# Optimization experiments

Hardware: AMD Instinct MI355X
Metric: run time of the kernel (lower is better)

## Reference

```python
import jax, jax.numpy as jnp
import numpy as np

B, N, DIM = 8, 1024, 768
HEADS, DHEAD = 12, 64
INNER = HEADS * DHEAD  # 768
ALPHA = 0.25
SCALE = DHEAD ** -0.5
EPS = 1e-5


def setup_inputs() -> dict:
    key = jax.random.key(0)
    ks = jax.random.split(key, 7)
    x = jax.random.normal(ks[0], (B, N, DIM), dtype=jnp.float32)
    h = jax.random.normal(ks[1], (B, HEADS, N, N), dtype=jnp.float32)
    gamma = jnp.ones((DIM,), dtype=jnp.float32)
    beta = jnp.zeros((DIM,), dtype=jnp.float32)
    w_qkv = jax.random.normal(ks[2], (DIM, 3 * INNER), dtype=jnp.float32) * (DIM ** -0.5)
    w_out = jax.random.normal(ks[3], (INNER, DIM), dtype=jnp.float32) * (INNER ** -0.5)
    b_out = jnp.zeros((DIM,), dtype=jnp.float32)
    return {"x": x, "h": h, "gamma": gamma, "beta": beta,
            "w_qkv": w_qkv, "w_out": w_out, "b_out": b_out}


def reference(x, h, gamma, beta, w_qkv, w_out, b_out):
    # LayerNorm over last dim
    mu = jnp.mean(x, axis=-1, keepdims=True)
    var = jnp.mean(jnp.square(x - mu), axis=-1, keepdims=True)
    xn = (x - mu) * jax.lax.rsqrt(var + EPS) * gamma + beta
    # fused QKV projection (no bias)
    qkv = xn @ w_qkv                                     # (b, n, 3*inner)
    q, k, v = jnp.split(qkv, 3, axis=-1)
    split_heads = lambda t: t.reshape(B, N, HEADS, DHEAD).transpose(0, 2, 1, 3)  # b h n d
    q, k, v = split_heads(q), split_heads(k), split_heads(v)
    raw = jnp.einsum('bhid,bhjd->bhij', q, k) * SCALE    # (b, h, n, n)
    blended = ALPHA * raw + (1.0 - ALPHA) * h
    attn = jax.nn.softmax(blended, axis=-1)              # dropout p=0 -> identity
    out = jnp.einsum('bhij,bhjd->bhid', attn, v)         # (b, h, n, d)
    out = out.transpose(0, 2, 1, 3).reshape(B, N, INNER)
    out = out @ w_out + b_out
    return (out, blended)
```

## Files before the change

### kernel.cpp

```cpp
#include <hip/hip_runtime.h>
#include <hip/hip_bf16.h>
#include <stdint.h>

#define NB 8
#define NSEQ 1024
#define DIMM 768
#define NHEADS 12
#define DH 64
#define NQKV 2304
#define ALPHA_ 0.25f
#define SCALE_ 0.125f
#define EPS_ 1e-5f

typedef __bf16 bf16;
typedef bf16 bf16x8 __attribute__((ext_vector_type(8)));
typedef bf16 bf16x4 __attribute__((ext_vector_type(4)));
typedef float f32x4 __attribute__((ext_vector_type(4)));

#define MFMA16(a, b, c) __builtin_amdgcn_mfma_f32_16x16x32_bf16((a), (b), (c), 0, 0, 0)

static __device__ __forceinline__ void load_lds16(const void* gsrc, void* ldst) {
  __builtin_amdgcn_global_load_lds(
      (__attribute__((address_space(1))) void*)gsrc,
      (__attribute__((address_space(3))) void*)ldst, 16, 0, 0);
}

#define BAR_LGKM()                                             \
  do {                                                         \
    __builtin_amdgcn_sched_barrier(0);                         \
    asm volatile("s_waitcnt lgkmcnt(0)" ::: "memory");         \
    __builtin_amdgcn_s_barrier();                              \
    __builtin_amdgcn_sched_barrier(0);                         \
  } while (0)

static __device__ __forceinline__ int swz(int row, int cb) {
  return cb ^ ((((row & 7) ^ ((cb >> 7) & 7)) << 4));
}

__global__ __launch_bounds__(256) void ln_kernel(
    const float* __restrict__ x, const float* __restrict__ gamma,
    const float* __restrict__ beta, bf16* __restrict__ xn) {
  const int row = blockIdx.x * 4 + (threadIdx.x >> 6);
  const int lane = threadIdx.x & 63;
  const float* xr = x + (size_t)row * DIMM;
  float4 v[3];
  float s = 0.f, s2 = 0.f;
#pragma unroll
  for (int c = 0; c < 3; ++c) {
    v[c] = *reinterpret_cast<const float4*>(xr + c * 256 + lane * 4);
    s += v[c].x + v[c].y + v[c].z + v[c].w;
    s2 += v[c].x * v[c].x + v[c].y * v[c].y + v[c].z * v[c].z + v[c].w * v[c].w;
  }
#pragma unroll
  for (int m = 1; m < 64; m <<= 1) {
    s += __shfl_xor(s, m);
    s2 += __shfl_xor(s2, m);
  }
  const float mu = s * (1.f / DIMM);
  const float rstd = rsqrtf(s2 * (1.f / DIMM) - mu * mu + EPS_);
#pragma unroll
  for (int c = 0; c < 3; ++c) {
    const float4 g4 = *reinterpret_cast<const float4*>(gamma + c * 256 + lane * 4);
    const float4 b4 = *reinterpret_cast<const float4*>(beta + c * 256 + lane * 4);
    bf16x4 o;
    o[0] = (bf16)((v[c].x - mu) * rstd * g4.x + b4.x);
    o[1] = (bf16)((v[c].y - mu) * rstd * g4.y + b4.y);
    o[2] = (bf16)((v[c].z - mu) * rstd * g4.z + b4.z);
    o[3] = (bf16)((v[c].w - mu) * rstd * g4.w + b4.w);
    *reinterpret_cast<bf16x4*>(xn + (size_t)row * DIMM + c * 256 + lane * 4) = o;
  }
}

__global__ __launch_bounds__(256) void tcast_kernel(
    const float* __restrict__ in, bf16* __restrict__ out, int R, int C) {
  __shared__ float tile[32][33];
  const int tx = threadIdx.x & 31, ty = threadIdx.x >> 5;
  const int c0 = blockIdx.x * 32, r0 = blockIdx.y * 32;
#pragma unroll
  for (int i = ty; i < 32; i += 8)
    tile[i][tx] = in[(size_t)(r0 + i) * C + c0 + tx];
  __syncthreads();
#pragma unroll
  for (int i = ty; i < 32; i += 8)
    out[(size_t)(c0 + i) * R + r0 + tx] = (bf16)tile[tx][i];
}

__global__ __launch_bounds__(256) void qkv_gemm(
    const bf16* __restrict__ xn, const bf16* __restrict__ wT,
    bf16* __restrict__ qb, bf16* __restrict__ kb, bf16* __restrict__ vt) {
  __shared__ __align__(16) bf16 As[128 * 32];
  __shared__ __align__(16) bf16 Bs[64 * 32];
  const int tid = threadIdx.x;
  const int wv = tid >> 6, l = tid & 63;
  const int l16 = l & 15, q4 = l >> 4;
  const int c0 = blockIdx.x * 64, row0 = blockIdx.y * 128;
  const int sr = tid >> 2, skk = (tid & 3) * 8;
  f32x4 acc0[4], acc1[4];
#pragma unroll
  for (int c = 0; c < 4; ++c) {
    acc0[c] = f32x4{0.f, 0.f, 0.f, 0.f};
    acc1[c] = f32x4{0.f, 0.f, 0.f, 0.f};
  }
  for (int k0 = 0; k0 < DIMM; k0 += 32) {
    __syncthreads();
    load_lds16(xn + (size_t)(row0 + sr) * DIMM + k0 + skk, As + tid * 8);
    load_lds16(xn + (size_t)(row0 + 64 + sr) * DIMM + k0 + skk, As + 2048 + tid * 8);
    load_lds16(wT + (size_t)(c0 + sr) * DIMM + k0 + skk, Bs + tid * 8);
    __syncthreads();
    const bf16x8 a0 = *reinterpret_cast<const bf16x8*>(&As[(wv * 32 + l16) * 32 + q4 * 8]);
    const bf16x8 a1 = *reinterpret_cast<const bf16x8*>(&As[(wv * 32 + 16 + l16) * 32 + q4 * 8]);
#pragma unroll
    for (int c = 0; c < 4; ++c) {
      const bf16x8 bb = *reinterpret_cast<const bf16x8*>(&Bs[(c * 16 + l16) * 32 + q4 * 8]);
      acc0[c] = MFMA16(a0, bb, acc0[c]);
      acc1[c] = MFMA16(a1, bb, acc1[c]);
    }
  }
  const int sect = c0 / DIMM;
  const int head = (c0 % DIMM) >> 6;
#pragma unroll
  for (int c = 0; c < 4; ++c) {
    const int dd = c * 16 + l16;
#pragma unroll
    for (int r = 0; r < 4; ++r) {
#pragma unroll
      for (int rsub = 0; rsub < 2; ++rsub) {
        const int gm = row0 + wv * 32 + rsub * 16 + q4 * 4 + r;
        const int b = gm >> 10, n = gm & 1023;
        const size_t bhh = (size_t)b * NHEADS + head;
        const float av = rsub ? acc1[c][r] : acc0[c][r];
        const bf16 val = (bf16)av;
        if (sect == 0)      qb[(bhh * NSEQ + n) * DH + dd] = val;
        else if (sect == 1) kb[(bhh * NSEQ + n) * DH + dd] = val;
        else                vt[(bhh * DH + dd) * NSEQ + n] = val;
      }
    }
  }
}

__global__ __launch_bounds__(256, 4) void attn_kernel(
    const bf16* __restrict__ qb, const bf16* __restrict__ kb,
    const bf16* __restrict__ vt, const float* __restrict__ h,
    float* __restrict__ blended, bf16* __restrict__ attn_out) {
  __shared__ __align__(16) char S_lds[16 * 1152];
  __shared__ __align__(16) float scl[16];
  __shared__ __align__(16) float lred[16];

  const int tid = threadIdx.x;
  const int wv = tid >> 6, l = tid & 63;
  const int l16 = l & 15, q4 = l >> 4;
  const int i0 = blockIdx.x * 16;
  const int bh = blockIdx.y;

  const float* hbase = h + ((size_t)bh << 20);
  float* bbase = blended + ((size_t)bh << 20);
  const bf16* kbase = kb + (size_t)bh * NSEQ * DH;
  const bf16* vbase = vt + (size_t)bh * DH * NSEQ;

  bf16x8 qT[2];
#pragma unroll
  for (int w2 = 0; w2 < 2; ++w2)
    qT[w2] = *reinterpret_cast<const bf16x8*>(
        qb + ((size_t)bh * NSEQ + i0 + l16) * DH + w2 * 32 + q4 * 8);

  f32x4 acc[4];
#pragma unroll
  for (int kk = 0; kk < 4; ++kk) acc[kk] = f32x4{0.f, 0.f, 0.f, 0.f};
  float m_run[4], l_run[4];
#pragma unroll
  for (int r = 0; r < 4; ++r) { m_run[r] = -1e30f; l_run[r] = 0.f; }

#pragma unroll
  for (int c = 0; c < 2; ++c) {
    {
      const bf16* kq = kbase + (size_t)(c * 512 + wv * 128 + l16) * DH + q4 * 8;
      char* srow_w = S_lds + l16 * 1152;
#pragma unroll
      for (int st = 0; st < 2; ++st) {
        f32x4 s[4];
#pragma unroll
        for (int js = 0; js < 4; ++js) s[js] = f32x4{0.f, 0.f, 0.f, 0.f};
#pragma unroll
        for (int js = 0; js < 4; ++js) {
#pragma unroll
          for (int w2 = 0; w2 < 2; ++w2) {
            const bf16x8 kf = *reinterpret_cast<const bf16x8*>(
                kq + (size_t)(st * 64 + js * 16) * DH + w2 * 32);
            s[js] = MFMA16(kf, qT[w2], s[js]);
          }
        }
#pragma unroll
        for (int js = 0; js < 4; ++js) {
          bf16x4 pk;
#pragma unroll
          for (int r = 0; r < 4; ++r) pk[r] = (bf16)(s[js][r] * (ALPHA_ * SCALE_));
          const int cb = (wv * 256 + st * 128 + js * 32 + q4 * 8);
          *reinterpret_cast<bf16x4*>(srow_w + swz(l16, cb)) = pk;
        }
      }
    }
    BAR_LGKM();

#pragma unroll
    for (int rr = 0; rr < 4; ++rr) {
      const int row = wv * 4 + rr;
      char* srow = S_lds + row * 1152;
      const bf16x8 sv = *reinterpret_cast<const bf16x8*>(srow + swz(row, l * 16));
      const float* hp = hbase + (size_t)(i0 + row) * NSEQ + c * 512 + l * 8;
      const f32x4 h0 = __builtin_nontemporal_load(reinterpret_cast<const f32x4*>(hp));
      const f32x4 h1 = __builtin_nontemporal_load(reinterpret_cast<const f32x4*>(hp + 4));
      float bl[8];
#pragma unroll
      for (int t = 0; t < 4; ++t) bl[t] = fmaf(0.75f, h0[t], (float)sv[t]);
#pragma unroll
      for (int t = 0; t < 4; ++t) bl[4 + t] = fmaf(0.75f, h1[t], (float)sv[4 + t]);
      float* bp = bbase + (size_t)(i0 + row) * NSEQ + c * 512 + l * 8;
      f32x4 b0, b1;
#pragma unroll
      for (int t = 0; t < 4; ++t) { b0[t] = bl[t]; b1[t] = bl[4 + t]; }
      __builtin_nontemporal_store(b0, reinterpret_cast<f32x4*>(bp));
      __builtin_nontemporal_store(b1, reinterpret_cast<f32x4*>(bp + 4));
      float tm = bl[0];
#pragma unroll
      for (int t = 1; t < 8; ++t) tm = fmaxf(tm, bl[t]);
#pragma unroll
      for (int mm = 1; mm < 64; mm <<= 1) tm = fmaxf(tm, __shfl_xor(tm, mm));
      const float mnew = fmaxf(m_run[rr], tm);
      const float sc = __expf(m_run[rr] - mnew);
      m_run[rr] = mnew;
      float rs = 0.f;
      bf16x8 pk;
#pragma unroll
      for (int t = 0; t < 8; ++t) {
        const float p = __expf(bl[t] - mnew);
        rs += p;
        pk[t] = (bf16)p;
      }
      *reinterpret_cast<bf16x8*>(srow + swz(row, l * 16)) = pk;
#pragma unroll
      for (int mm = 1; mm < 64; mm <<= 1) rs += __shfl_xor(rs, mm);
      l_run[rr] = l_run[rr] * sc + rs;
      if (l == 0) {
        scl[row] = sc;
        if (c == 1) lred[row] = l_run[rr];
      }
    }
    BAR_LGKM();

    {
      const f32x4 sclv = *reinterpret_cast<const f32x4*>(&scl[q4 * 4]);
      const bf16* vq = vbase + (size_t)(wv * 16 + l16) * NSEQ + c * 512 + q4 * 8;
      char* prow = S_lds + l16 * 1152;
#pragma unroll
      for (int kk = 0; kk < 4; ++kk) acc[kk] *= sclv;
#pragma unroll
      for (int kk = 0; kk < 4; ++kk) {
#pragma unroll
        for (int ki = 0; ki < 4; ++ki) {
          const int ks = kk * 4 + ki;
          const bf16x8 pa = *reinterpret_cast<const bf16x8*>(
              prow + swz(l16, ks * 64 + q4 * 16));
          const bf16x8 vf = *reinterpret_cast<const bf16x8*>(vq + ks * 32);
          acc[kk] = MFMA16(pa, vf, acc[kk]);
        }
      }
    }
    if (c == 0) BAR_LGKM();
  }

  const f32x4 lv = *reinterpret_cast<const f32x4*>(&lred[q4 * 4]);
  const f32x4 af = (acc[0] + acc[1]) + (acc[2] + acc[3]);
  const int b = bh / NHEADS, head = bh % NHEADS;
#pragma unroll
  for (int r = 0; r < 4; ++r) {
    const int q = q4 * 4 + r;
    attn_out[((size_t)b * NSEQ + i0 + q) * DIMM + head * DH + wv * 16 + l16] =
        (bf16)(af[r] / lv[r]);
  }
}

__global__ __launch_bounds__(256) void oproj_gemm(
    const bf16* __restrict__ ain, const bf16* __restrict__ wT,
    const float* __restrict__ bias, float* __restrict__ out) {
  __shared__ __align__(16) bf16 As[128 * 32];
  __shared__ __align__(16) bf16 Bs[64 * 32];
  const int tid = threadIdx.x;
  const int wv = tid >> 6, l = tid & 63;
  const int l16 = l & 15, q4 = l >> 4;
  const int c0 = blockIdx.x * 64, row0 = blockIdx.y * 128;
  const int sr = tid >> 2, skk = (tid & 3) * 8;
  f32x4 acc0[4], acc1[4];
#pragma unroll
  for (int c = 0; c < 4; ++c) {
    acc0[c] = f32x4{0.f, 0.f, 0.f, 0.f};
    acc1[c] = f32x4{0.f, 0.f, 0.f, 0.f};
  }
  for (int k0 = 0; k0 < DIMM; k0 += 32) {
    __syncthreads();
    load_lds16(ain + (size_t)(row0 + sr) * DIMM + k0 + skk, As + tid * 8);
    load_lds16(ain + (size_t)(row0 + 64 + sr) * DIMM + k0 + skk, As + 2048 + tid * 8);
    load_lds16(wT + (size_t)(c0 + sr) * DIMM + k0 + skk, Bs + tid * 8);
    __syncthreads();
    const bf16x8 a0 = *reinterpret_cast<const bf16x8*>(&As[(wv * 32 + l16) * 32 + q4 * 8]);
    const bf16x8 a1 = *reinterpret_cast<const bf16x8*>(&As[(wv * 32 + 16 + l16) * 32 + q4 * 8]);
#pragma unroll
    for (int c = 0; c < 4; ++c) {
      const bf16x8 bb = *reinterpret_cast<const bf16x8*>(&Bs[(c * 16 + l16) * 32 + q4 * 8]);
      acc0[c] = MFMA16(a0, bb, acc0[c]);
      acc1[c] = MFMA16(a1, bb, acc1[c]);
    }
  }
#pragma unroll
  for (int c = 0; c < 4; ++c) {
    const int gc = c0 + c * 16 + l16;
    const float bv = bias[gc];
#pragma unroll
    for (int r = 0; r < 4; ++r) {
      out[(size_t)(row0 + wv * 32 + q4 * 4 + r) * DIMM + gc] = acc0[c][r] + bv;
      out[(size_t)(row0 + wv * 32 + 16 + q4 * 4 + r) * DIMM + gc] = acc1[c][r] + bv;
    }
  }
}

extern "C" void kernel_launch(void* const* d_in, const int* in_sizes, int n_in,
                              void* d_out, int out_size, void* d_ws, size_t ws_size,
                              hipStream_t stream) {
  const float* x = (const float*)d_in[0];
  const float* h = (const float*)d_in[1];
  const float* gamma = (const float*)d_in[2];
  const float* beta = (const float*)d_in[3];
  const float* w_qkv = (const float*)d_in[4];
  const float* w_out = (const float*)d_in[5];
  const float* b_out = (const float*)d_in[6];
  float* out = (float*)d_out;
  float* blended = out + (size_t)NB * NSEQ * DIMM;

  char* ws = (char*)d_ws;
  bf16* xn = (bf16*)(ws);
  bf16* qb = (bf16*)(ws + 12582912);
  bf16* kb = (bf16*)(ws + 25165824);
  bf16* vt = (bf16*)(ws + 37748736);
  bf16* wqkvT = (bf16*)(ws + 50331648);
  bf16* woutT = (bf16*)(ws + 53870592);

  hipLaunchKernelGGL(ln_kernel, dim3(2048), dim3(256), 0, stream, x, gamma, beta, xn);
  hipLaunchKernelGGL(tcast_kernel, dim3(72, 24), dim3(256), 0, stream, w_qkv, wqkvT, DIMM, NQKV);
  hipLaunchKernelGGL(tcast_kernel, dim3(24, 24), dim3(256), 0, stream, w_out, woutT, DIMM, DIMM);
  hipLaunchKernelGGL(qkv_gemm, dim3(36, 64), dim3(256), 0, stream, xn, wqkvT, qb, kb, vt);
  hipLaunchKernelGGL(attn_kernel, dim3(64, 96), dim3(256), 0, stream, qb, kb, vt, h, blended, xn);
  hipLaunchKernelGGL(oproj_gemm, dim3(12, 64), dim3(256), 0, stream, xn, woutT, b_out, out);
}
```

Baseline: 430.0 us.

## Process two query tiles per attention block with software-pipelined phases

Each attention block now handles 32 query rows as two 16-row tiles with separate LDS score buffers. The QK^T, softmax/blend, and PV phases of the two tiles are interleaved, so one tile's memory-bound h/blended pass can overlap the other tile's MFMA work, and the number of barriers per tile drops. The h loads and blended stores also change from nontemporal to plain accesses. In exchange the block doubles its LDS use and register state, and the launch bound drops from 4 to 3 blocks per CU, which may lower occupancy.

```diff
diff --git a/kernel.cpp b/kernel.cpp
--- a/kernel.cpp
+++ b/kernel.cpp
@@ -138,18 +138,18 @@
   }
 }
 
-__global__ __launch_bounds__(256, 4) void attn_kernel(
+__global__ __launch_bounds__(256, 3) void attn_kernel(
     const bf16* __restrict__ qb, const bf16* __restrict__ kb,
     const bf16* __restrict__ vt, const float* __restrict__ h,
     float* __restrict__ blended, bf16* __restrict__ attn_out) {
-  __shared__ __align__(16) char S_lds[16 * 1152];
-  __shared__ __align__(16) float scl[16];
-  __shared__ __align__(16) float lred[16];
+  __shared__ __align__(16) char S_lds[2 * 16 * 1152];
+  __shared__ __align__(16) float scl[2][16];
+  __shared__ __align__(16) float lred[2][16];
 
   const int tid = threadIdx.x;
   const int wv = tid >> 6, l = tid & 63;
   const int l16 = l & 15, q4 = l >> 4;
-  const int i0 = blockIdx.x * 16;
+  const int i0 = blockIdx.x * 32;
   const int bh = blockIdx.y;
 
   const float* hbase = h + ((size_t)bh << 20);
@@ -157,72 +157,77 @@
   const bf16* kbase = kb + (size_t)bh * NSEQ * DH;
   const bf16* vbase = vt + (size_t)bh * DH * NSEQ;
 
-  bf16x8 qT[2];
-#pragma unroll
-  for (int w2 = 0; w2 < 2; ++w2)
-    qT[w2] = *reinterpret_cast<const bf16x8*>(
+  bf16x8 qTA[2], qTB[2];
+#pragma unroll
+  for (int w2 = 0; w2 < 2; ++w2) {
+    qTA[w2] = *reinterpret_cast<const bf16x8*>(
         qb + ((size_t)bh * NSEQ + i0 + l16) * DH + w2 * 32 + q4 * 8);
-
-  f32x4 acc[4];
-#pragma unroll
-  for (int kk = 0; kk < 4; ++kk) acc[kk] = f32x4{0.f, 0.f, 0.f, 0.f};
-  float m_run[4], l_run[4];
-#pragma unroll
-  for (int r = 0; r < 4; ++r) { m_run[r] = -1e30f; l_run[r] = 0.f; }
-
-#pragma unroll
-  for (int c = 0; c < 2; ++c) {
-    {
-      const bf16* kq = kbase + (size_t)(c * 512 + wv * 128 + l16) * DH + q4 * 8;
-      char* srow_w = S_lds + l16 * 1152;
-#pragma unroll
-      for (int st = 0; st < 2; ++st) {
-        f32x4 s[4];
-#pragma unroll
-        for (int js = 0; js < 4; ++js) s[js] = f32x4{0.f, 0.f, 0.f, 0.f};
-#pragma unroll
-        for (int js = 0; js < 4; ++js) {
-#pragma unroll
-          for (int w2 = 0; w2 < 2; ++w2) {
-            const bf16x8 kf = *reinterpret_cast<const bf16x8*>(
-                kq + (size_t)(st * 64 + js * 16) * DH + w2 * 32);
-            s[js] = MFMA16(kf, qT[w2], s[js]);
-          }
+    qTB[w2] = *reinterpret_cast<const bf16x8*>(
+        qb + ((size_t)bh * NSEQ + i0 + 16 + l16) * DH + w2 * 32 + q4 * 8);
+  }
+
+  f32x4 accA[4], accB[4];
+  float mA[4], lA[4], mB[4], lB[4];
+#pragma unroll
+  for (int k = 0; k < 4; ++k) {
+    accA[k] = f32x4{0.f, 0.f, 0.f, 0.f};
+    accB[k] = f32x4{0.f, 0.f, 0.f, 0.f};
+    mA[k] = -1e30f; lA[k] = 0.f; mB[k] = -1e30f; lB[k] = 0.f;
+  }
+
+  auto P1 = [&](int t, int c, const bf16x8 (&qT)[2]) {
+    const bf16* kq = kbase + (size_t)(c * 512 + wv * 128 + l16) * DH + q4 * 8;
+    char* srow_w = S_lds + t * 18432 + l16 * 1152;
+#pragma unroll
+    for (int st = 0; st < 2; ++st) {
+      f32x4 s[4];
+#pragma unroll
+      for (int js = 0; js < 4; ++js) s[js] = f32x4{0.f, 0.f, 0.f, 0.f};
+#pragma unroll
+      for (int js = 0; js < 4; ++js) {
+#pragma unroll
+        for (int w2 = 0; w2 < 2; ++w2) {
+          const bf16x8 kf = *reinterpret_cast<const bf16x8*>(
+              kq + (size_t)(st * 64 + js * 16) * DH + w2 * 32);
+          s[js] = MFMA16(kf, qT[w2], s[js]);
         }
-#pragma unroll
-        for (int js = 0; js < 4; ++js) {
-          bf16x4 pk;
-#pragma unroll
-          for (int r = 0; r < 4; ++r) pk[r] = (bf16)(s[js][r] * (ALPHA_ * SCALE_));
-          const int cb = (wv * 256 + st * 128 + js * 32 + q4 * 8);
-          *reinterpret_cast<bf16x4*>(srow_w + swz(l16, cb)) = pk;
-        }
-      }
-    }
-    BAR_LGKM();
-
+      }
+#pragma unroll
+      for (int js = 0; js < 4; ++js) {
+        bf16x4 pk;
+#pragma unroll
+        for (int r = 0; r < 4; ++r) pk[r] = (bf16)(s[js][r] * (ALPHA_ * SCALE_));
+        const int cb = (wv * 256 + st * 128 + js * 32 + q4 * 8);
+        *reinterpret_cast<bf16x4*>(srow_w + swz(l16, cb)) = pk;
+      }
+    }
+  };
+
+  auto P2 = [&](int t, int c, float (&m_run)[4], float (&l_run)[4]) {
+    char* sreg = S_lds + t * 18432;
+    const int gi0 = i0 + t * 16;
 #pragma unroll
     for (int rr = 0; rr < 4; ++rr) {
       const int row = wv * 4 + rr;
-      char* srow = S_lds + row * 1152;
+      char* srow = sreg + row * 1152;
       const bf16x8 sv = *reinterpret_cast<const bf16x8*>(srow + swz(row, l * 16));
-      const float* hp = hbase + (size_t)(i0 + row) * NSEQ + c * 512 + l * 8;
-      const f32x4 h0 = __builtin_nontemporal_load(reinterpret_cast<const f32x4*>(hp));
-      const f32x4 h1 = __builtin_nontemporal_load(reinterpret_cast<const f32x4*>(hp + 4));
+      const float* hp = hbase + (size_t)(gi0 + row) * NSEQ + c * 512 + l * 8;
+      const f32x4 h0 = *reinterpret_cast<const f32x4*>(hp);
+      const f32x4 h1 = *reinterpret_cast<const f32x4*>(hp + 4);
       float bl[8];
 #pragma unroll
-      for (int t = 0; t < 4; ++t) bl[t] = fmaf(0.75f, h0[t], (float)sv[t]);
-#pragma unroll
-      for (int t = 0; t < 4; ++t) bl[4 + t] = fmaf(0.75f, h1[t], (float)sv[4 + t]);
-      float* bp = bbase + (size_t)(i0 + row) * NSEQ + c * 512 + l * 8;
+      for (int u = 0; u < 4; ++u) bl[u] = fmaf(0.75f, h0[u], (float)sv[u]);
+#pragma unroll
+      for (int u = 0; u < 4; ++u) bl[4 + u] = fmaf(0.75f, h1[u], (float)sv[4 + u]);
+      float* bp = bbase + (size_t)(gi0 + row) * NSEQ + c * 512 + l * 8;
       f32x4 b0, b1;
 #pragma unroll
-      for (int t = 0; t < 4; ++t) { b0[t] = bl[t]; b1[t] = bl[4 + t]; }
-      __builtin_nontemporal_store(b0, reinterpret_cast<f32x4*>(bp));
-      __builtin_nontemporal_store(b1, reinterpret_cast<f32x4*>(bp + 4));
+      for (int u = 0; u < 4; ++u) { b0[u] = bl[u]; b1[u] = bl[4 + u]; }
+      *reinterpret_cast<f32x4*>(bp) = b0;
+      *reinterpret_cast<f32x4*>(bp + 4) = b1;
       float tm = bl[0];
 #pragma unroll
-      for (int t = 1; t < 8; ++t) tm = fmaxf(tm, bl[t]);
+      for (int u = 1; u < 8; ++u) tm = fmaxf(tm, bl[u]);
 #pragma unroll
       for (int mm = 1; mm < 64; mm <<= 1) tm = fmaxf(tm, __shfl_xor(tm, mm));
       const float mnew = fmaxf(m_run[rr], tm);
@@ -231,51 +236,75 @@
       float rs = 0.f;
       bf16x8 pk;
 #pragma unroll
-      for (int t = 0; t < 8; ++t) {
-        const float p = __expf(bl[t] - mnew);
+      for (int u = 0; u < 8; ++u) {
+        const float p = __expf(bl[u] - mnew);
         rs += p;
-        pk[t] = (bf16)p;
+        pk[u] = (bf16)p;
       }
       *reinterpret_cast<bf16x8*>(srow + swz(row, l * 16)) = pk;
 #pragma unroll
       for (int mm = 1; mm < 64; mm <<= 1) rs += __shfl_xor(rs, mm);
       l_run[rr] = l_run[rr] * sc + rs;
       if (l == 0) {
-        scl[row] = sc;
-        if (c == 1) lred[row] = l_run[rr];
-      }
-    }
-    BAR_LGKM();
-
-    {
-      const f32x4 sclv = *reinterpret_cast<const f32x4*>(&scl[q4 * 4]);
-      const bf16* vq = vbase + (size_t)(wv * 16 + l16) * NSEQ + c * 512 + q4 * 8;
-      char* prow = S_lds + l16 * 1152;
-#pragma unroll
-      for (int kk = 0; kk < 4; ++kk) acc[kk] *= sclv;
-#pragma unroll
-      for (int kk = 0; kk < 4; ++kk) {
-#pragma unroll
-        for (int ki = 0; ki < 4; ++ki) {
-          const int ks = kk * 4 + ki;
-          const bf16x8 pa = *reinterpret_cast<const bf16x8*>(
-              prow + swz(l16, ks * 64 + q4 * 16));
-          const bf16x8 vf = *reinterpret_cast<const bf16x8*>(vq + ks * 32);
-          acc[kk] = MFMA16(pa, vf, acc[kk]);
-        }
-      }
-    }
-    if (c == 0) BAR_LGKM();
-  }
-
-  const f32x4 lv = *reinterpret_cast<const f32x4*>(&lred[q4 * 4]);
-  const f32x4 af = (acc[0] + acc[1]) + (acc[2] + acc[3]);
+        scl[t][row] = sc;
+        if (c == 1) lred[t][row] = l_run[rr];
+      }
+    }
+  };
+
+  auto P3 = [&](int t, int c, f32x4 (&acc)[4]) {
+    const f32x4 sclv = *reinterpret_cast<const f32x4*>(&scl[t][q4 * 4]);
+    const bf16* vq = vbase + (size_t)(wv * 16 + l16) * NSEQ + c * 512 + q4 * 8;
+    char* prow = S_lds + t * 18432 + l16 * 1152;
+#pragma unroll
+    for (int kk = 0; kk < 4; ++kk) acc[kk] *= sclv;
+#pragma unroll
+    for (int kk = 0; kk < 4; ++kk) {
+#pragma unroll
+      for (int ki = 0; ki < 4; ++ki) {
+        const int ks = kk * 4 + ki;
+        const bf16x8 pa = *reinterpret_cast<const bf16x8*>(
+            prow + swz(l16, ks * 64 + q4 * 16));
+        const bf16x8 vf = *reinterpret_cast<const bf16x8*>(vq + ks * 32);
+        acc[kk] = MFMA16(pa, vf, acc[kk]);
+      }
+    }
+  };
+
+  P1(0, 0, qTA);
+  BAR_LGKM();
+  P2(0, 0, mA, lA);  P1(1, 0, qTB);
+  BAR_LGKM();
+  P2(1, 0, mB, lB);  P3(0, 0, accA);
+  BAR_LGKM();
+  P1(0, 1, qTA);     P3(1, 0, accB);
+  BAR_LGKM();
+  P2(0, 1, mA, lA);  P1(1, 1, qTB);
+  BAR_LGKM();
+  P2(1, 1, mB, lB);  P3(0, 1, accA);
+  BAR_LGKM();
+  P3(1, 1, accB);
+
   const int b = bh / NHEADS, head = bh % NHEADS;
-#pragma unroll
-  for (int r = 0; r < 4; ++r) {
-    const int q = q4 * 4 + r;
-    attn_out[((size_t)b * NSEQ + i0 + q) * DIMM + head * DH + wv * 16 + l16] =
-        (bf16)(af[r] / lv[r]);
+  {
+    const f32x4 lv = *reinterpret_cast<const f32x4*>(&lred[0][q4 * 4]);
+    const f32x4 af = (accA[0] + accA[1]) + (accA[2] + accA[3]);
+#pragma unroll
+    for (int r = 0; r < 4; ++r) {
+      const int q = q4 * 4 + r;
+      attn_out[((size_t)b * NSEQ + i0 + q) * DIMM + head * DH + wv * 16 + l16] =
+          (bf16)(af[r] / lv[r]);
+    }
+  }
+  {
+    const f32x4 lv = *reinterpret_cast<const f32x4*>(&lred[1][q4 * 4]);
+    const f32x4 af = (accB[0] + accB[1]) + (accB[2] + accB[3]);
+#pragma unroll
+    for (int r = 0; r < 4; ++r) {
+      const int q = q4 * 4 + r;
+      attn_out[((size_t)b * NSEQ + i0 + 16 + q) * DIMM + head * DH + wv * 16 + l16] =
+          (bf16)(af[r] / lv[r]);
+    }
   }
 }
 
@@ -347,6 +376,6 @@
   hipLaunchKernelGGL(tcast_kernel, dim3(72, 24), dim3(256), 0, stream, w_qkv, wqkvT, DIMM, NQKV);
   hipLaunchKernelGGL(tcast_kernel, dim3(24, 24), dim3(256), 0, stream, w_out, woutT, DIMM, DIMM);
   hipLaunchKernelGGL(qkv_gemm, dim3(36, 64), dim3(256), 0, stream, xn, wqkvT, qb, kb, vt);
-  hipLaunchKernelGGL(attn_kernel, dim3(64, 96), dim3(256), 0, stream, qb, kb, vt, h, blended, xn);
+  hipLaunchKernelGGL(attn_kernel, dim3(32, 96), dim3(256), 0, stream, qb, kb, vt, h, blended, xn);
   hipLaunchKernelGGL(oproj_gemm, dim3(12, 64), dim3(256), 0, stream, xn, woutT, b_out, out);
 }
```

Result: faster. 413.2 us (-3.9%).
